# Kernel tuning notes

Hardware: AMD Instinct MI355X
Metric: run time of the kernel (lower is better)

Reference implementation:

```python
import jax, jax.numpy as jnp
import numpy as np

NBINS = 256


def _normalized_histogram(x, nbins=NBINS):
    # x: [B, H, W, 3] floats in [0, 1]
    # TF histogram_fixed_width binning rule over value_range [0, 1]:
    #   idx = clip(int(x * nbins), 0, nbins - 1)
    idx = jnp.clip((x * nbins).astype(jnp.int32), 0, nbins - 1)  # [B,H,W,3]
    # Fuse all 3 channels into one scatter-add: flat bin id = c*nbins + idx
    chan_offset = jnp.arange(3, dtype=jnp.int32) * nbins  # [3]
    flat = (idx + chan_offset).ravel()  # [B*H*W*3]
    counts = jax.ops.segment_sum(
        jnp.ones_like(flat, dtype=jnp.float32), flat, num_segments=3 * nbins
    ).reshape(3, nbins)  # [3, nbins]
    # Normalize each channel histogram to sum to 1, stack channels last -> [nbins, 3]
    hist = counts / jnp.sum(counts, axis=1, keepdims=True)
    return hist.T


def setup_inputs() -> dict:
    key = jax.random.key(0)
    inputs = jax.random.uniform(key, (64, 512, 512, 3), dtype=jnp.float32)
    return {"inputs": inputs}


def reference(inputs):
    return _normalized_histogram(inputs, NBINS)
```

## Files before the change

### kernel.cpp

```cpp
#include <hip/hip_runtime.h>

#define NBINS 256
#define NCH 3
#define HSIZE (NBINS * NCH)
#define NWAVE 4
#define SLOTS 8
#define TPB 256
#define BLOCKS 2048

typedef float f4 __attribute__((ext_vector_type(4)));

__global__ __launch_bounds__(TPB) void hist_kernel(const float* __restrict__ in,
                                                   unsigned int* __restrict__ ws,
                                                   int n) {
    __shared__ unsigned int lds[NWAVE][HSIZE];

    const int tid = threadIdx.x;

    unsigned int* flat = &lds[0][0];
    #pragma unroll
    for (int i = 0; i < NWAVE * HSIZE / TPB; ++i)
        flat[tid + i * TPB] = 0u;
    __syncthreads();

    unsigned int* h = lds[tid >> 6];

    const long long ngrp   = n / 12;
    const long long stride = (long long)gridDim.x * TPB;
    const f4* __restrict__ in4 = (const f4*)in;

    #pragma unroll 2
    for (long long g = (long long)blockIdx.x * TPB + tid; g < ngrp; g += stride) {
        const f4* p = in4 + 3 * g;
        f4 a = __builtin_nontemporal_load(p + 0);
        f4 b = __builtin_nontemporal_load(p + 1);
        f4 c = __builtin_nontemporal_load(p + 2);

        int a0 = min(max((int)(a.x * 256.0f), 0), 255);
        int a1 = min(max((int)(a.y * 256.0f), 0), 255);
        int a2 = min(max((int)(a.z * 256.0f), 0), 255);
        int a3 = min(max((int)(a.w * 256.0f), 0), 255);
        int b0 = min(max((int)(b.x * 256.0f), 0), 255);
        int b1 = min(max((int)(b.y * 256.0f), 0), 255);
        int b2 = min(max((int)(b.z * 256.0f), 0), 255);
        int b3 = min(max((int)(b.w * 256.0f), 0), 255);
        int c0 = min(max((int)(c.x * 256.0f), 0), 255);
        int c1 = min(max((int)(c.y * 256.0f), 0), 255);
        int c2 = min(max((int)(c.z * 256.0f), 0), 255);
        int c3 = min(max((int)(c.w * 256.0f), 0), 255);

        atomicAdd(&h[0 * NBINS + a0], 1u);
        atomicAdd(&h[1 * NBINS + a1], 1u);
        atomicAdd(&h[2 * NBINS + a2], 1u);
        atomicAdd(&h[0 * NBINS + a3], 1u);
        atomicAdd(&h[1 * NBINS + b0], 1u);
        atomicAdd(&h[2 * NBINS + b1], 1u);
        atomicAdd(&h[0 * NBINS + b2], 1u);
        atomicAdd(&h[1 * NBINS + b3], 1u);
        atomicAdd(&h[2 * NBINS + c0], 1u);
        atomicAdd(&h[0 * NBINS + c1], 1u);
        atomicAdd(&h[1 * NBINS + c2], 1u);
        atomicAdd(&h[2 * NBINS + c3], 1u);
    }

    if (blockIdx.x == 0) {
        for (long long e = ngrp * 12 + tid; e < n; e += TPB) {
            float x = in[e];
            int bin = min(max((int)(x * 256.0f), 0), 255);
            int ch = (int)(e % 3);
            atomicAdd(&h[ch * NBINS + bin], 1u);
        }
    }

    __syncthreads();

    unsigned int* dst = ws + (blockIdx.x & (SLOTS - 1)) * HSIZE;
    #pragma unroll
    for (int i = 0; i < HSIZE / TPB; ++i) {
        int idx = tid + i * TPB;
        unsigned int s = lds[0][idx] + lds[1][idx] + lds[2][idx] + lds[3][idx];
        if (s) atomicAdd(&dst[idx], s);
    }
}

__global__ void finalize_kernel(const unsigned int* __restrict__ ws,
                                float* __restrict__ out,
                                float total) {
    int t = threadIdx.x;
    int bin = t / 3;
    int c = t - 3 * bin;
    unsigned int s = 0;
    #pragma unroll
    for (int k = 0; k < SLOTS; ++k)
        s += ws[k * HSIZE + c * NBINS + bin];
    out[t] = (float)s / total;
}

extern "C" void kernel_launch(void* const* d_in, const int* in_sizes, int n_in,
                              void* d_out, int out_size, void* d_ws, size_t ws_size,
                              hipStream_t stream) {
    const float* in = (const float*)d_in[0];
    const int n = in_sizes[0];
    unsigned int* ws = (unsigned int*)d_ws;

    hipMemsetAsync(ws, 0, SLOTS * HSIZE * sizeof(unsigned int), stream);
    hist_kernel<<<BLOCKS, TPB, 0, stream>>>(in, ws, n);
    finalize_kernel<<<1, HSIZE, 0, stream>>>(ws, (float*)d_out, (float)(n / NCH));
}
```

Measured before the change: 270.0 us.

## Replace global atomic merge with per-block partials and multi-block float-atomic reduce

Each histogram block now writes its own partial histogram to a separate workspace row instead of atomically adding into 8 shared slots. A new 32-block reduce kernel sums those rows and float-atomically accumulates normalized values into the zeroed output. The input loads also switch from nontemporal to ordinary loads. This removes global atomic contention at the end of the histogram kernel, at the cost of a 6 MB workspace round trip and floating-point atomics whose summation order is nondeterministic.

```diff
diff --git a/kernel.cpp b/kernel.cpp
--- a/kernel.cpp
+++ b/kernel.cpp
@@ -4,9 +4,9 @@
 #define NCH 3
 #define HSIZE (NBINS * NCH)
 #define NWAVE 4
-#define SLOTS 8
 #define TPB 256
 #define BLOCKS 2048
+#define RBLOCKS 32
 
 typedef float f4 __attribute__((ext_vector_type(4)));
 
@@ -32,9 +32,9 @@
     #pragma unroll 2
     for (long long g = (long long)blockIdx.x * TPB + tid; g < ngrp; g += stride) {
         const f4* p = in4 + 3 * g;
-        f4 a = __builtin_nontemporal_load(p + 0);
-        f4 b = __builtin_nontemporal_load(p + 1);
-        f4 c = __builtin_nontemporal_load(p + 2);
+        f4 a = p[0];
+        f4 b = p[1];
+        f4 c = p[2];
 
         int a0 = min(max((int)(a.x * 256.0f), 0), 255);
         int a1 = min(max((int)(a.y * 256.0f), 0), 255);
@@ -74,26 +74,39 @@
 
     __syncthreads();
 
-    unsigned int* dst = ws + (blockIdx.x & (SLOTS - 1)) * HSIZE;
+    unsigned int* dst = ws + (long long)blockIdx.x * HSIZE;
     #pragma unroll
     for (int i = 0; i < HSIZE / TPB; ++i) {
         int idx = tid + i * TPB;
-        unsigned int s = lds[0][idx] + lds[1][idx] + lds[2][idx] + lds[3][idx];
-        if (s) atomicAdd(&dst[idx], s);
+        dst[idx] = lds[0][idx] + lds[1][idx] + lds[2][idx] + lds[3][idx];
     }
 }
 
-__global__ void finalize_kernel(const unsigned int* __restrict__ ws,
-                                float* __restrict__ out,
-                                float total) {
-    int t = threadIdx.x;
-    int bin = t / 3;
-    int c = t - 3 * bin;
-    unsigned int s = 0;
-    #pragma unroll
-    for (int k = 0; k < SLOTS; ++k)
-        s += ws[k * HSIZE + c * NBINS + bin];
-    out[t] = (float)s / total;
+__global__ __launch_bounds__(TPB) void reduce_kernel(const unsigned int* __restrict__ ws,
+                                                     float* __restrict__ out,
+                                                     float inv_total) {
+    const int tid = threadIdx.x;
+    const int row0 = blockIdx.x * (BLOCKS / RBLOCKS);
+
+    unsigned int s0 = 0, s1 = 0, s2 = 0;
+    for (int r = 0; r < BLOCKS / RBLOCKS; ++r) {
+        const unsigned int* rowp = ws + (long long)(row0 + r) * HSIZE;
+        s0 += rowp[tid];
+        s1 += rowp[tid + 256];
+        s2 += rowp[tid + 512];
+    }
+    {
+        int idx = tid;
+        atomicAdd(&out[(idx & 255) * 3 + (idx >> 8)], (float)s0 * inv_total);
+    }
+    {
+        int idx = tid + 256;
+        atomicAdd(&out[(idx & 255) * 3 + (idx >> 8)], (float)s1 * inv_total);
+    }
+    {
+        int idx = tid + 512;
+        atomicAdd(&out[(idx & 255) * 3 + (idx >> 8)], (float)s2 * inv_total);
+    }
 }
 
 extern "C" void kernel_launch(void* const* d_in, const int* in_sizes, int n_in,
@@ -102,8 +115,9 @@
     const float* in = (const float*)d_in[0];
     const int n = in_sizes[0];
     unsigned int* ws = (unsigned int*)d_ws;
+    float* out = (float*)d_out;
 
-    hipMemsetAsync(ws, 0, SLOTS * HSIZE * sizeof(unsigned int), stream);
+    hipMemsetAsync(out, 0, HSIZE * sizeof(float), stream);
     hist_kernel<<<BLOCKS, TPB, 0, stream>>>(in, ws, n);
-    finalize_kernel<<<1, HSIZE, 0, stream>>>(ws, (float*)d_out, (float)(n / NCH));
+    reduce_kernel<<<RBLOCKS, TPB, 0, stream>>>(ws, out, 1.0f / (float)(n / NCH));
 }
```

Measured after the change: 279.0 us. 3.3% more time.

## Fuse finalize into histogram kernel via last-block reduction; use regular loads

Applied to the files above, without the earlier changes.

Removes the separate finalize kernel launch. Each block bumps a completion counter after flushing its partial histogram, and the last block to finish sums the slots and writes the normalized output. Input loads also switch from nontemporal to ordinary vector loads. This trades a kernel launch for a device-scope fence and atomic per block plus a serial tail in one block. The division by total becomes a multiply by its reciprocal, which may differ in rounding.

```diff
diff --git a/kernel.cpp b/kernel.cpp
--- a/kernel.cpp
+++ b/kernel.cpp
@@ -12,8 +12,10 @@
 
 __global__ __launch_bounds__(TPB) void hist_kernel(const float* __restrict__ in,
                                                    unsigned int* __restrict__ ws,
-                                                   int n) {
+                                                   float* __restrict__ out,
+                                                   int n, float inv_total) {
     __shared__ unsigned int lds[NWAVE][HSIZE];
+    __shared__ int is_last;
 
     const int tid = threadIdx.x;
 
@@ -32,9 +34,9 @@
     #pragma unroll 2
     for (long long g = (long long)blockIdx.x * TPB + tid; g < ngrp; g += stride) {
         const f4* p = in4 + 3 * g;
-        f4 a = __builtin_nontemporal_load(p + 0);
-        f4 b = __builtin_nontemporal_load(p + 1);
-        f4 c = __builtin_nontemporal_load(p + 2);
+        f4 a = p[0];
+        f4 b = p[1];
+        f4 c = p[2];
 
         int a0 = min(max((int)(a.x * 256.0f), 0), 255);
         int a1 = min(max((int)(a.y * 256.0f), 0), 255);
@@ -81,19 +83,27 @@
         unsigned int s = lds[0][idx] + lds[1][idx] + lds[2][idx] + lds[3][idx];
         if (s) atomicAdd(&dst[idx], s);
     }
-}
 
-__global__ void finalize_kernel(const unsigned int* __restrict__ ws,
-                                float* __restrict__ out,
-                                float total) {
-    int t = threadIdx.x;
-    int bin = t / 3;
-    int c = t - 3 * bin;
-    unsigned int s = 0;
-    #pragma unroll
-    for (int k = 0; k < SLOTS; ++k)
-        s += ws[k * HSIZE + c * NBINS + bin];
-    out[t] = (float)s / total;
+    __threadfence();
+    if (tid == 0) {
+        unsigned int prev = atomicAdd(&ws[SLOTS * HSIZE], 1u);
+        is_last = (prev == (unsigned int)(gridDim.x - 1));
+    }
+    __syncthreads();
+
+    if (is_last) {
+        __threadfence();
+        #pragma unroll
+        for (int i = 0; i < HSIZE / TPB; ++i) {
+            int idx = tid + i * TPB;
+            unsigned int s = 0;
+            #pragma unroll
+            for (int k = 0; k < SLOTS; ++k)
+                s += atomicAdd(&ws[k * HSIZE + idx], 0u);
+            int c = idx >> 8, bin = idx & 255;
+            out[bin * 3 + c] = (float)s * inv_total;
+        }
+    }
 }
 
 extern "C" void kernel_launch(void* const* d_in, const int* in_sizes, int n_in,
@@ -103,7 +113,7 @@
     const int n = in_sizes[0];
     unsigned int* ws = (unsigned int*)d_ws;
 
-    hipMemsetAsync(ws, 0, SLOTS * HSIZE * sizeof(unsigned int), stream);
-    hist_kernel<<<BLOCKS, TPB, 0, stream>>>(in, ws, n);
-    finalize_kernel<<<1, HSIZE, 0, stream>>>(ws, (float*)d_out, (float)(n / NCH));
+    hipMemsetAsync(ws, 0, (SLOTS * HSIZE + 1) * sizeof(unsigned int), stream);
+    hist_kernel<<<BLOCKS, TPB, 0, stream>>>(in, ws, (float*)d_out, n,
+                                            1.0f / (float)(n / NCH));
 }
```

Result: slower. 563.8 us (+108.8%).
